# Kernel tuning notes

Measured on AMD Instinct MI355X. Metric: run time of the kernel, lower is better.

Reference implementation:

```python
import jax, jax.numpy as jnp
import numpy as np

B, L, E, H = 2, 2048, 1024, 16
D = E // H

def setup_inputs() -> dict:
    key = jax.random.key(0)
    ks = jax.random.split(key, 6)
    s = 1.0 / np.sqrt(E)
    return {
        "x": jax.random.normal(ks[0], (B, L, E), dtype=jnp.float32),
        "attention_mask": jnp.ones((B, L), dtype=jnp.float32),
        "Wq": jax.random.normal(ks[1], (E, E), dtype=jnp.float32) * s,
        "Wk": jax.random.normal(ks[2], (E, E), dtype=jnp.float32) * s,
        "Wv": jax.random.normal(ks[3], (E, E), dtype=jnp.float32) * s,
        "Wo": jax.random.normal(ks[4], (E, E), dtype=jnp.float32) * s,
        "bo": jnp.zeros((E,), dtype=jnp.float32),
    }

def reference(x, attention_mask, Wq, Wk, Wv, Wo, bo):
    b, l, e = x.shape
    h, d = H, D

    def proj(W):
        # (B,L,E) @ (E,E)^T -> (B,L,E) -> (B,H,L,D)
        return (x @ W.T).reshape(b, l, h, d).transpose(0, 2, 1, 3)

    q, k, v = proj(Wq), proj(Wk), proj(Wv)

    # multiplicative attention mask on q, k, v (mask shape (B,L) -> (B,1,L,1))
    m = attention_mask[:, None, :, None].astype(x.dtype)
    q, k, v = q * m, k * m, v * m

    scale = 1.0 / np.sqrt(d)
    scores = jnp.einsum('bhqd,bhkd->bhqk', q, k) * scale  # (B,H,L,L)
    causal = jnp.tril(jnp.ones((l, l), dtype=bool))
    scores = jnp.where(causal[None, None], scores, -jnp.inf)
    attn = jax.nn.softmax(scores, axis=-1)
    y = jnp.einsum('bhqk,bhkd->bhqd', attn, v)  # (B,H,L,D)
    y = y.transpose(0, 2, 1, 3).reshape(b, l, e)
    return y @ Wo.T + bo
```

## Files before the change

kernel.cpp:

```cpp
#include <hip/hip_runtime.h>
#include <cstdint>
#include <cstddef>
#include <math.h>

#define BB 2
#define LL 2048
#define EE 1024
#define HH 16
#define DD 64
#define MM (BB*LL)

typedef short short8 __attribute__((ext_vector_type(8)));
typedef float f32x4 __attribute__((ext_vector_type(4)));
typedef float f32x16 __attribute__((ext_vector_type(16)));

#define GPTR __attribute__((address_space(1)))
#define LPTR __attribute__((address_space(3)))

__device__ __forceinline__ unsigned pk_bf16(float lo, float hi) {
  unsigned r;
  asm("v_cvt_pk_bf16_f32 %0, %1, %2" : "=v"(r) : "v"(lo), "v"(hi));
  return r;
}
__device__ __forceinline__ unsigned short f32_bf16(float f) {
  return (unsigned short)pk_bf16(f, f);
}
__device__ __forceinline__ float ex2(float x) {
  float r;
  asm("v_exp_f32 %0, %1" : "=v"(r) : "v"(x));
  return r;
}
__device__ __forceinline__ void swap32(unsigned &a, unsigned &b) {
  asm("v_permlane32_swap_b32 %0, %1" : "+v"(a), "+v"(b));
}
__device__ __forceinline__ float xh_max(float v) {
  union { float f; unsigned u; } a, b;
  a.f = v;
  asm("v_mov_b32 %0, %1" : "=&v"(b.u) : "v"(a.u));
  asm("v_permlane32_swap_b32 %0, %1" : "+v"(a.u), "+v"(b.u));
  return fmaxf(a.f, b.f);
}
__device__ __forceinline__ float xh_sum(float v) {
  union { float f; unsigned u; } a, b;
  a.f = v;
  asm("v_mov_b32 %0, %1" : "=&v"(b.u) : "v"(a.u));
  asm("v_permlane32_swap_b32 %0, %1" : "+v"(a.u), "+v"(b.u));
  return a.f + b.f;
}
__device__ __forceinline__ f32x16 zero16() {
  f32x16 v;
  #pragma unroll
  for (int e = 0; e < 16; ++e) v[e] = 0.f;
  return v;
}

__global__ void cvt_all(const float* __restrict__ x,  const float* __restrict__ wq,
                        const float* __restrict__ wk, const float* __restrict__ wv,
                        const float* __restrict__ wo,
                        unsigned short* __restrict__ xb,  unsigned short* __restrict__ wqb,
                        unsigned short* __restrict__ wkb, unsigned short* __restrict__ wvb,
                        unsigned short* __restrict__ wob)
{
  int i = (blockIdx.x * 256 + threadIdx.x) * 4;
  if (i >= MM * EE + 4 * EE * EE) return;
  const float* s; unsigned short* d; int off;
  if (i < MM * EE) { s = x; d = xb; off = i; }
  else {
    int k = i - MM * EE;
    int w = k >> 20;
    off = k & (EE * EE - 1);
    s = (w == 0) ? wq : (w == 1) ? wk : (w == 2) ? wv : wo;
    d = (w == 0) ? wqb : (w == 1) ? wkb : (w == 2) ? wvb : wob;
  }
  float4 v = *(const float4*)(s + off);
  uint2 o;
  o.x = pk_bf16(v.x, v.y);
  o.y = pk_bf16(v.z, v.w);
  *(uint2*)(d + off) = o;
}

template<int MODE>
__global__ __launch_bounds__(256, 3)
void gemm128(const unsigned short* __restrict__ A,
             const unsigned short* __restrict__ W0,
             const unsigned short* __restrict__ W1,
             const unsigned short* __restrict__ W2,
             const float* __restrict__ mask,
             const float* __restrict__ bias,
             unsigned short* __restrict__ O0,
             unsigned short* __restrict__ O1,
             unsigned short* __restrict__ O2,
             float* __restrict__ OF)
{
  constexpr int K = EE;
  const int tid = threadIdx.x;
  const int lane = tid & 63;
  const int wid = tid >> 6;
  const int g = lane >> 4, li = lane & 15;
  const int m0 = blockIdx.y * 128;
  const int n0 = blockIdx.x * 128;
  const int z = blockIdx.z;

  const unsigned short* Wp = W0;
  if (MODE == 0) Wp = (z == 0) ? W0 : ((z == 1) ? W1 : W2);

  __shared__ unsigned short As[128 * 64];
  __shared__ unsigned short Bs[128 * 64];

  f32x4 acc[4][4];
  f32x4 zero = {0.f, 0.f, 0.f, 0.f};
  #pragma unroll
  for (int i = 0; i < 4; ++i)
    #pragma unroll
    for (int j = 0; j < 4; ++j) acc[i][j] = zero;

  const int wm = (wid >> 1) * 64;
  const int wn = (wid & 1) * 64;

  for (int kt = 0; kt < K; kt += 64) {
    #pragma unroll
    for (int j = 0; j < 4; ++j) {
      int c = j * 256 + tid;
      int row = c >> 3;
      int lcol = ((c & 7) * 16) ^ ((row & 7) << 4);
      __builtin_amdgcn_global_load_lds(
        (const GPTR void*)((const char*)(A + (size_t)(m0 + row) * K + kt) + lcol),
        (LPTR void*)((char*)As + c * 16), 16, 0, 0);
      __builtin_amdgcn_global_load_lds(
        (const GPTR void*)((const char*)(Wp + (size_t)(n0 + row) * K + kt) + lcol),
        (LPTR void*)((char*)Bs + c * 16), 16, 0, 0);
    }
    __syncthreads();

    #pragma unroll
    for (int kk = 0; kk < 2; ++kk) {
      short8 a[4], b[4];
      const int colb = (kk * 32 + g * 8) * 2;
      #pragma unroll
      for (int i = 0; i < 4; ++i) {
        int ar = wm + i * 16 + li;
        a[i] = *(const short8*)((const char*)As + ar * 128 + (colb ^ ((ar & 7) << 4)));
        int br = wn + i * 16 + li;
        b[i] = *(const short8*)((const char*)Bs + br * 128 + (colb ^ ((br & 7) << 4)));
      }
      #pragma unroll
      for (int i = 0; i < 4; ++i)
        #pragma unroll
        for (int j = 0; j < 4; ++j)
          acc[i][j] = __builtin_amdgcn_mfma_f32_16x16x32_bf16(a[i], b[j], acc[i][j], 0, 0, 0);
    }
    __syncthreads();
  }

  if (MODE == 0) {
    if (z == 2) {
      #pragma unroll
      for (int i = 0; i < 4; ++i) {
        int mbase = m0 + wm + i * 16 + g * 4;
        int bb2 = mbase >> 11;
        int l0  = mbase & (LL - 1);
        float mk[4];
        #pragma unroll
        for (int r = 0; r < 4; ++r) mk[r] = mask[mbase + r];
        #pragma unroll
        for (int j = 0; j < 4; ++j) {
          int n = n0 + wn + j * 16 + li;
          int h2 = n >> 6, dd2 = n & 63;
          uint2 o;
          o.x = pk_bf16(acc[i][j][0] * mk[0], acc[i][j][1] * mk[1]);
          o.y = pk_bf16(acc[i][j][2] * mk[2], acc[i][j][3] * mk[3]);
          size_t off = (size_t)(bb2 * HH + h2) * (LL * DD)
                     + (size_t)(l0 >> 5) * (DD * 32) + dd2 * 32 + (l0 & 31);
          *(uint2*)(O2 + off) = o;
        }
      }
    } else {
      unsigned short* Op = (z == 0) ? O0 : O1;
      const float sc = (z == 0) ? 0.125f * 1.44269504088896f : 1.0f;
      #pragma unroll
      for (int i = 0; i < 4; ++i) {
        #pragma unroll
        for (int r = 0; r < 4; ++r) {
          int m = m0 + wm + i * 16 + g * 4 + r;
          float mk = mask[m] * sc;
          int bb = m >> 11;
          int l  = m & (LL - 1);
          #pragma unroll
          for (int j = 0; j < 4; ++j) {
            int n = n0 + wn + j * 16 + li;
            int h = n >> 6, d = n & 63;
            size_t off = (((size_t)(bb * HH + h)) * LL + l) * DD + d;
            Op[off] = f32_bf16(acc[i][j][r] * mk);
          }
        }
      }
    }
  } else {
    #pragma unroll
    for (int i = 0; i < 4; ++i) {
      #pragma unroll
      for (int j = 0; j < 4; ++j) {
        int n = n0 + wn + j * 16 + li;
        float bv = bias[n];
        #pragma unroll
        for (int r = 0; r < 4; ++r) {
          int m = m0 + wm + i * 16 + g * 4 + r;
          OF[(size_t)m * EE + n] = acc[i][j][r] + bv;
        }
      }
    }
  }
}

__global__ __launch_bounds__(128, 2)
void attn11(const unsigned short* __restrict__ Q,
            const unsigned short* __restrict__ K,
            const unsigned short* __restrict__ VT,
            unsigned short* __restrict__ Y)
{
  const int tid = threadIdx.x, lane = tid & 63, w = tid >> 6;
  const int l31 = lane & 31, hi = lane >> 5;

  const int id = blockIdx.x;
  const int lo = id & 7;
  const int r_ = id >> 3;
  const int bh = (r_ & 3) * 8 + lo;
  const int p  = r_ >> 2;
  const int qth = 63 - p;
  const int qtl = p;
  const int b = bh >> 4, h = bh & (HH - 1);
  const size_t kbase = (size_t)bh * LL * DD;

  const unsigned short* Kg  = K + kbase;
  const unsigned short* VTg = VT + kbase;

  const int qrh = qth * 32 + l31;
  const int qrl = qtl * 32 + l31;

  short8 qfh[4], qfl[4];
  {
    const unsigned short* Qr = Q + kbase + (size_t)qrh * DD + hi * 8;
    #pragma unroll
    for (int kc = 0; kc < 4; ++kc) qfh[kc] = *(const short8*)(Qr + kc * 16);
    const unsigned short* Qs = Q + kbase + (size_t)qrl * DD + hi * 8;
    #pragma unroll
    for (int kc = 0; kc < 4; ++kc) qfl[kc] = *(const short8*)(Qs + kc * 16);
  }

  const f32x16 kZero = zero16();
  f32x16 oh0 = zero16(), oh1 = zero16(), ol0 = zero16(), ol1 = zero16();
  float mh = -INFINITY, ml = -INFINITY;
  float lsh4[4] = {0.f, 0.f, 0.f, 0.f};
  float lsl4[4] = {0.f, 0.f, 0.f, 0.f};

  short8 kA[4], vA[4], kB[4], vB[4];

  auto loadtile = [&](short8 (&kk)[4], short8 (&vv)[4], int t2) {
    const int kv0 = t2 << 5;
    const unsigned short* Kp = Kg + ((size_t)(kv0 + l31) << 6) + hi * 8;
    #pragma unroll
    for (int kc = 0; kc < 4; ++kc) kk[kc] = *(const short8*)(Kp + kc * 16);
    const unsigned short* Vp = VTg + (size_t)(kv0 >> 5) * (DD * 32) + l31 * 32 + hi * 8;
    vv[0] = *(const short8*)(Vp);
    vv[1] = *(const short8*)(Vp + 16);
    vv[2] = *(const short8*)(Vp + 32 * 32);
    vv[3] = *(const short8*)(Vp + 32 * 32 + 16);
  };

  loadtile(kA, vA, w);

  auto qk = [&](const short8 (&ck)[4], const short8 (&qf)[4]) -> f32x16 {
    f32x16 s0 = __builtin_amdgcn_mfma_f32_32x32x16_bf16(ck[0], qf[0], kZero, 0, 0, 0);
    f32x16 s1 = __builtin_amdgcn_mfma_f32_32x32x16_bf16(ck[1], qf[1], kZero, 0, 0, 0);
    s0 = __builtin_amdgcn_mfma_f32_32x32x16_bf16(ck[2], qf[2], s0, 0, 0, 0);
    s1 = __builtin_amdgcn_mfma_f32_32x32x16_bf16(ck[3], qf[3], s1, 0, 0, 0);
    #pragma unroll
    for (int e = 0; e < 16; ++e) s0[e] += s1[e];
    return s0;
  };

  auto diagmask = [&](f32x16 &s) {
    #pragma unroll
    for (int i = 0; i < 16; ++i) {
      int kvr = (i & 3) + 8 * (i >> 2) + 4 * hi;
      if (kvr > l31) s[i] = -INFINITY;
    }
  };

  auto process = [&](f32x16 &s, const short8 (&cv)[4],
                     float &mq, float (&ls4)[4], f32x16 &o0, f32x16 &o1) {
    float r0 = fmaxf(fmaxf(fmaxf(s[0], s[8]),  fmaxf(s[1], s[9])),  fmaxf(s[2], s[10]));
    float r1 = fmaxf(fmaxf(fmaxf(s[3], s[11]), fmaxf(s[4], s[12])), fmaxf(s[5], s[13]));
    float r2 = fmaxf(fmaxf(s[6], s[14]), fmaxf(s[7], s[15]));
    float mv = fmaxf(fmaxf(r0, r1), r2);

    if (!__all(mv <= mq + 8.0f)) {
      float mnew = fmaxf(mq, xh_max(mv));
      float al = ex2(mq - mnew);
      mq = mnew;
      #pragma unroll
      for (int e = 0; e < 16; ++e) { o0[e] *= al; o1[e] *= al; }
      #pragma unroll
      for (int e = 0; e < 4; ++e) ls4[e] *= al;
    }

    #pragma unroll
    for (int e = 0; e < 16; ++e) s[e] = ex2(s[e] - mq);
    ls4[0] += (s[0] + s[8])  + (s[4] + s[12]);
    ls4[1] += (s[1] + s[9])  + (s[5] + s[13]);
    ls4[2] += (s[2] + s[10]) + (s[6] + s[14]);
    ls4[3] += (s[3] + s[11]) + (s[7] + s[15]);

    auto mkfrag = [&](int base) -> short8 {
      unsigned a0 = pk_bf16(s[base + 0], s[base + 1]);
      unsigned a1 = pk_bf16(s[base + 2], s[base + 3]);
      unsigned b0 = pk_bf16(s[base + 4], s[base + 5]);
      unsigned b1 = pk_bf16(s[base + 6], s[base + 7]);
      swap32(a0, b0);
      swap32(a1, b1);
      union { unsigned u[4]; short8 s8; } f;
      f.u[0] = a0; f.u[1] = a1; f.u[2] = b0; f.u[3] = b1;
      return f.s8;
    };
    short8 pf0 = mkfrag(0), pf1 = mkfrag(8);

    o0 = __builtin_amdgcn_mfma_f32_32x32x16_bf16(cv[0], pf0, o0, 0, 0, 0);
    o1 = __builtin_amdgcn_mfma_f32_32x32x16_bf16(cv[2], pf0, o1, 0, 0, 0);
    o0 = __builtin_amdgcn_mfma_f32_32x32x16_bf16(cv[1], pf1, o0, 0, 0, 0);
    o1 = __builtin_amdgcn_mfma_f32_32x32x16_bf16(cv[3], pf1, o1, 0, 0, 0);
  };

  auto body = [&](short8 (&ck)[4], short8 (&cv)[4],
                  short8 (&nk)[4], short8 (&nv)[4], int t) {
    if (t + 2 <= qth) loadtile(nk, nv, t + 2);

    if (t <= qtl) {
      f32x16 sh = qk(ck, qfh);
      f32x16 sl = qk(ck, qfl);
      if (t == qtl) diagmask(sl);
      process(sh, cv, mh, lsh4, oh0, oh1);
      process(sl, cv, ml, lsl4, ol0, ol1);
    } else {
      f32x16 sh = qk(ck, qfh);
      if (t == qth) diagmask(sh);
      process(sh, cv, mh, lsh4, oh0, oh1);
    }
  };

  for (int t = w; t <= qth; t += 4) {
    body(kA, vA, kB, vB, t);
    if (t + 2 <= qth) body(kB, vB, kA, vA, t + 2);
  }

  float lsh = (lsh4[0] + lsh4[1]) + (lsh4[2] + lsh4[3]);
  float lsl = (lsl4[0] + lsl4[1]) + (lsl4[2] + lsl4[3]);

  __shared__ float mg[2][64][34];
  if (w == 1) {
    mg[0][lane][0] = mh; mg[0][lane][1] = lsh;
    mg[1][lane][0] = ml; mg[1][lane][1] = lsl;
    #pragma unroll
    for (int e = 0; e < 16; ++e) {
      mg[0][lane][2 + e] = oh0[e]; mg[0][lane][18 + e] = oh1[e];
      mg[1][lane][2 + e] = ol0[e]; mg[1][lane][18 + e] = ol1[e];
    }
  }
  __syncthreads();
  if (w == 0) {
    #pragma unroll
    for (int q = 0; q < 2; ++q) {
      float mw = (q == 0) ? mh : ml;
      float lw = (q == 0) ? lsh : lsl;
      const f32x16& o0 = (q == 0) ? oh0 : ol0;
      const f32x16& o1 = (q == 0) ? oh1 : ol1;
      int qrow = (q == 0) ? qrh : qrl;
      float m1 = mg[q][lane][0], l1 = mg[q][lane][1];
      float M = fmaxf(mw, m1);
      float a0 = ex2(fmaxf(mw - M, -200.0f));
      float a1 = ex2(fmaxf(m1 - M, -200.0f));
      float LtH = lw * a0 + l1 * a1;
      float Lt = xh_sum(LtH);
      float inv = 1.0f / Lt;
      unsigned short* Yr = Y + ((size_t)b * LL + qrow) * EE + h * DD;
      #pragma unroll
      for (int rg = 0; rg < 4; ++rg) {
        uint2 u0, u1;
        int i = rg * 4;
        u0.x = pk_bf16((o0[i]     * a0 + mg[q][lane][2 + i]     * a1) * inv,
                       (o0[i + 1] * a0 + mg[q][lane][3 + i]     * a1) * inv);
        u0.y = pk_bf16((o0[i + 2] * a0 + mg[q][lane][4 + i]     * a1) * inv,
                       (o0[i + 3] * a0 + mg[q][lane][5 + i]     * a1) * inv);
        u1.x = pk_bf16((o1[i]     * a0 + mg[q][lane][18 + i]    * a1) * inv,
                       (o1[i + 1] * a0 + mg[q][lane][19 + i]    * a1) * inv);
        u1.y = pk_bf16((o1[i + 2] * a0 + mg[q][lane][20 + i]    * a1) * inv,
                       (o1[i + 3] * a0 + mg[q][lane][21 + i]    * a1) * inv);
        *(uint2*)(Yr + rg * 8 + hi * 4) = u0;
        *(uint2*)(Yr + 32 + rg * 8 + hi * 4) = u1;
      }
    }
  }
}

extern "C" void kernel_launch(void* const* d_in, const int* in_sizes, int n_in,
                              void* d_out, int out_size, void* d_ws, size_t ws_size,
                              hipStream_t stream) {
  const float* x    = (const float*)d_in[0];
  const float* mask = (const float*)d_in[1];
  const float* Wq   = (const float*)d_in[2];
  const float* Wk   = (const float*)d_in[3];
  const float* Wv   = (const float*)d_in[4];
  const float* Wo   = (const float*)d_in[5];
  const float* bo   = (const float*)d_in[6];
  float* out = (float*)d_out;

  char* ws = (char*)d_ws;
  unsigned short* xb  = (unsigned short*)(ws);
  unsigned short* wqb = (unsigned short*)(ws + ((size_t)8  << 20));
  unsigned short* wkb = (unsigned short*)(ws + ((size_t)10 << 20));
  unsigned short* wvb = (unsigned short*)(ws + ((size_t)12 << 20));
  unsigned short* wob = (unsigned short*)(ws + ((size_t)14 << 20));
  unsigned short* Qb  = (unsigned short*)(ws + ((size_t)16 << 20));
  unsigned short* Kb  = (unsigned short*)(ws + ((size_t)24 << 20));
  unsigned short* VTb = (unsigned short*)(ws + ((size_t)32 << 20));
  unsigned short* Yb  = (unsigned short*)(ws + ((size_t)40 << 20));

  cvt_all<<<8192, 256, 0, stream>>>(x, Wq, Wk, Wv, Wo, xb, wqb, wkb, wvb, wob);

  gemm128<0><<<dim3(EE / 128, MM / 128, 3), 256, 0, stream>>>(
      xb, wqb, wkb, wvb, mask, nullptr, Qb, Kb, VTb, nullptr);

  attn11<<<dim3(1024), 128, 0, stream>>>(Qb, Kb, VTb, Yb);

  gemm128<1><<<dim3(EE / 128, MM / 128, 1), 256, 0, stream>>>(
      Yb, wob, nullptr, nullptr, nullptr, bo, nullptr, nullptr, nullptr, out);
}
```

Measured before the change: 107.4 us.

## Process two KV tiles per softmax update and split K/V prefetch in attention

The attention loop now handles the two KV tiles (t and t+2) together for the high query row. It does one combined max check and rescale, then issues eight PV MFMAs back to back. K and V loads for the next pair are split and placed around the softmax work, so K arrives before V is needed and loads overlap the exp/MFMA work. This halves the online-softmax rescale checks for the long row and deepens prefetch. The cost is more live registers (two score tiles plus four fragment sets), which may add register pressure under the 2-wave launch bound.

```diff
diff --git a/kernel.cpp b/kernel.cpp
--- a/kernel.cpp
+++ b/kernel.cpp
@@ -213,7 +213,7 @@
 }
 
 __global__ __launch_bounds__(128, 2)
-void attn11(const unsigned short* __restrict__ Q,
+void attn14(const unsigned short* __restrict__ Q,
             const unsigned short* __restrict__ K,
             const unsigned short* __restrict__ VT,
             unsigned short* __restrict__ Y)
@@ -255,11 +255,14 @@
 
   short8 kA[4], vA[4], kB[4], vB[4];
 
-  auto loadtile = [&](short8 (&kk)[4], short8 (&vv)[4], int t2) {
+  auto loadK = [&](short8 (&kk)[4], int t2) {
     const int kv0 = t2 << 5;
     const unsigned short* Kp = Kg + ((size_t)(kv0 + l31) << 6) + hi * 8;
     #pragma unroll
     for (int kc = 0; kc < 4; ++kc) kk[kc] = *(const short8*)(Kp + kc * 16);
+  };
+  auto loadV = [&](short8 (&vv)[4], int t2) {
+    const int kv0 = t2 << 5;
     const unsigned short* Vp = VTg + (size_t)(kv0 >> 5) * (DD * 32) + l31 * 32 + hi * 8;
     vv[0] = *(const short8*)(Vp);
     vv[1] = *(const short8*)(Vp + 16);
@@ -267,8 +270,6 @@
     vv[3] = *(const short8*)(Vp + 32 * 32 + 16);
   };
 
-  loadtile(kA, vA, w);
-
   auto qk = [&](const short8 (&ck)[4], const short8 (&qf)[4]) -> f32x16 {
     f32x16 s0 = __builtin_amdgcn_mfma_f32_32x32x16_bf16(ck[0], qf[0], kZero, 0, 0, 0);
     f32x16 s1 = __builtin_amdgcn_mfma_f32_32x32x16_bf16(ck[1], qf[1], kZero, 0, 0, 0);
@@ -287,13 +288,28 @@
     }
   };
 
-  auto process = [&](f32x16 &s, const short8 (&cv)[4],
-                     float &mq, float (&ls4)[4], f32x16 &o0, f32x16 &o1) {
+  auto localmax = [&](const f32x16 &s) -> float {
     float r0 = fmaxf(fmaxf(fmaxf(s[0], s[8]),  fmaxf(s[1], s[9])),  fmaxf(s[2], s[10]));
     float r1 = fmaxf(fmaxf(fmaxf(s[3], s[11]), fmaxf(s[4], s[12])), fmaxf(s[5], s[13]));
     float r2 = fmaxf(fmaxf(s[6], s[14]), fmaxf(s[7], s[15]));
-    float mv = fmaxf(fmaxf(r0, r1), r2);
-
+    return fmaxf(fmaxf(r0, r1), r2);
+  };
+
+  auto mkfrag = [&](const f32x16 &s, int base) -> short8 {
+    unsigned a0 = pk_bf16(s[base + 0], s[base + 1]);
+    unsigned a1 = pk_bf16(s[base + 2], s[base + 3]);
+    unsigned b0 = pk_bf16(s[base + 4], s[base + 5]);
+    unsigned b1 = pk_bf16(s[base + 6], s[base + 7]);
+    swap32(a0, b0);
+    swap32(a1, b1);
+    union { unsigned u[4]; short8 s8; } f;
+    f.u[0] = a0; f.u[1] = a1; f.u[2] = b0; f.u[3] = b1;
+    return f.s8;
+  };
+
+  auto process = [&](f32x16 &s, const short8 (&cv)[4],
+                     float &mq, float (&ls4)[4], f32x16 &o0, f32x16 &o1) {
+    float mv = localmax(s);
     if (!__all(mv <= mq + 8.0f)) {
       float mnew = fmaxf(mq, xh_max(mv));
       float al = ex2(mq - mnew);
@@ -303,53 +319,87 @@
       #pragma unroll
       for (int e = 0; e < 4; ++e) ls4[e] *= al;
     }
-
     #pragma unroll
     for (int e = 0; e < 16; ++e) s[e] = ex2(s[e] - mq);
     ls4[0] += (s[0] + s[8])  + (s[4] + s[12]);
     ls4[1] += (s[1] + s[9])  + (s[5] + s[13]);
     ls4[2] += (s[2] + s[10]) + (s[6] + s[14]);
     ls4[3] += (s[3] + s[11]) + (s[7] + s[15]);
-
-    auto mkfrag = [&](int base) -> short8 {
-      unsigned a0 = pk_bf16(s[base + 0], s[base + 1]);
-      unsigned a1 = pk_bf16(s[base + 2], s[base + 3]);
-      unsigned b0 = pk_bf16(s[base + 4], s[base + 5]);
-      unsigned b1 = pk_bf16(s[base + 6], s[base + 7]);
-      swap32(a0, b0);
-      swap32(a1, b1);
-      union { unsigned u[4]; short8 s8; } f;
-      f.u[0] = a0; f.u[1] = a1; f.u[2] = b0; f.u[3] = b1;
-      return f.s8;
-    };
-    short8 pf0 = mkfrag(0), pf1 = mkfrag(8);
-
+    short8 pf0 = mkfrag(s, 0), pf1 = mkfrag(s, 8);
     o0 = __builtin_amdgcn_mfma_f32_32x32x16_bf16(cv[0], pf0, o0, 0, 0, 0);
     o1 = __builtin_amdgcn_mfma_f32_32x32x16_bf16(cv[2], pf0, o1, 0, 0, 0);
     o0 = __builtin_amdgcn_mfma_f32_32x32x16_bf16(cv[1], pf1, o0, 0, 0, 0);
     o1 = __builtin_amdgcn_mfma_f32_32x32x16_bf16(cv[3], pf1, o1, 0, 0, 0);
   };
 
-  auto body = [&](short8 (&ck)[4], short8 (&cv)[4],
-                  short8 (&nk)[4], short8 (&nv)[4], int t) {
-    if (t + 2 <= qth) loadtile(nk, nv, t + 2);
+  auto process2 = [&](f32x16 &sa, f32x16 &sb) {
+    float mv = fmaxf(localmax(sa), localmax(sb));
+    if (!__all(mv <= mh + 8.0f)) {
+      float mnew = fmaxf(mh, xh_max(mv));
+      float al = ex2(mh - mnew);
+      mh = mnew;
+      #pragma unroll
+      for (int e = 0; e < 16; ++e) { oh0[e] *= al; oh1[e] *= al; }
+      #pragma unroll
+      for (int e = 0; e < 4; ++e) lsh4[e] *= al;
+    }
+    #pragma unroll
+    for (int e = 0; e < 16; ++e) sa[e] = ex2(sa[e] - mh);
+    #pragma unroll
+    for (int e = 0; e < 16; ++e) sb[e] = ex2(sb[e] - mh);
+    lsh4[0] += (sa[0] + sa[8])  + (sa[4] + sa[12]) + (sb[0] + sb[8])  + (sb[4] + sb[12]);
+    lsh4[1] += (sa[1] + sa[9])  + (sa[5] + sa[13]) + (sb[1] + sb[9])  + (sb[5] + sb[13]);
+    lsh4[2] += (sa[2] + sa[10]) + (sa[6] + sa[14]) + (sb[2] + sb[10]) + (sb[6] + sb[14]);
+    lsh4[3] += (sa[3] + sa[11]) + (sa[7] + sa[15]) + (sb[3] + sb[11]) + (sb[7] + sb[15]);
+    short8 pa0 = mkfrag(sa, 0), pa1 = mkfrag(sa, 8);
+    short8 pb0 = mkfrag(sb, 0), pb1 = mkfrag(sb, 8);
+    oh0 = __builtin_amdgcn_mfma_f32_32x32x16_bf16(vA[0], pa0, oh0, 0, 0, 0);
+    oh1 = __builtin_amdgcn_mfma_f32_32x32x16_bf16(vA[2], pa0, oh1, 0, 0, 0);
+    oh0 = __builtin_amdgcn_mfma_f32_32x32x16_bf16(vA[1], pa1, oh0, 0, 0, 0);
+    oh1 = __builtin_amdgcn_mfma_f32_32x32x16_bf16(vA[3], pa1, oh1, 0, 0, 0);
+    oh0 = __builtin_amdgcn_mfma_f32_32x32x16_bf16(vB[0], pb0, oh0, 0, 0, 0);
+    oh1 = __builtin_amdgcn_mfma_f32_32x32x16_bf16(vB[2], pb0, oh1, 0, 0, 0);
+    oh0 = __builtin_amdgcn_mfma_f32_32x32x16_bf16(vB[1], pb1, oh0, 0, 0, 0);
+    oh1 = __builtin_amdgcn_mfma_f32_32x32x16_bf16(vB[3], pb1, oh1, 0, 0, 0);
+  };
+
+  loadK(kA, w);  loadV(vA, w);
+  loadK(kB, w + 2); loadV(vB, w + 2);
+
+  int t = w;
+  for (; t + 2 <= qth; t += 4) {
+    f32x16 sa = qk(kA, qfh);
+    f32x16 sb = qk(kB, qfh);
+    if (t + 2 == qth) diagmask(sb);
 
     if (t <= qtl) {
-      f32x16 sh = qk(ck, qfh);
-      f32x16 sl = qk(ck, qfl);
+      f32x16 sl = qk(kA, qfl);
       if (t == qtl) diagmask(sl);
-      process(sh, cv, mh, lsh4, oh0, oh1);
-      process(sl, cv, ml, lsl4, ol0, ol1);
-    } else {
-      f32x16 sh = qk(ck, qfh);
-      if (t == qth) diagmask(sh);
-      process(sh, cv, mh, lsh4, oh0, oh1);
-    }
-  };
-
-  for (int t = w; t <= qth; t += 4) {
-    body(kA, vA, kB, vB, t);
-    if (t + 2 <= qth) body(kB, vB, kA, vA, t + 2);
+      process(sl, vA, ml, lsl4, ol0, ol1);
+    }
+    if (t + 2 <= qtl) {
+      f32x16 sl = qk(kB, qfl);
+      if (t + 2 == qtl) diagmask(sl);
+      process(sl, vB, ml, lsl4, ol0, ol1);
+    }
+
+    if (t + 4 <= qth) loadK(kA, t + 4);
+    if (t + 6 <= qth) loadK(kB, t + 6);
+
+    process2(sa, sb);
+
+    if (t + 4 <= qth) loadV(vA, t + 4);
+    if (t + 6 <= qth) loadV(vB, t + 6);
+  }
+  if (t <= qth) {
+    f32x16 sh = qk(kA, qfh);
+    if (t == qth) diagmask(sh);
+    if (t <= qtl) {
+      f32x16 sl = qk(kA, qfl);
+      if (t == qtl) diagmask(sl);
+      process(sl, vA, ml, lsl4, ol0, ol1);
+    }
+    process(sh, vA, mh, lsh4, oh0, oh1);
   }
 
   float lsh = (lsh4[0] + lsh4[1]) + (lsh4[2] + lsh4[3]);
@@ -386,14 +436,14 @@
       for (int rg = 0; rg < 4; ++rg) {
         uint2 u0, u1;
         int i = rg * 4;
-        u0.x = pk_bf16((o0[i]     * a0 + mg[q][lane][2 + i]     * a1) * inv,
-                       (o0[i + 1] * a0 + mg[q][lane][3 + i]     * a1) * inv);
-        u0.y = pk_bf16((o0[i + 2] * a0 + mg[q][lane][4 + i]     * a1) * inv,
-                       (o0[i + 3] * a0 + mg[q][lane][5 + i]     * a1) * inv);
-        u1.x = pk_bf16((o1[i]     * a0 + mg[q][lane][18 + i]    * a1) * inv,
-                       (o1[i + 1] * a0 + mg[q][lane][19 + i]    * a1) * inv);
-        u1.y = pk_bf16((o1[i + 2] * a0 + mg[q][lane][20 + i]    * a1) * inv,
-                       (o1[i + 3] * a0 + mg[q][lane][21 + i]    * a1) * inv);
+        u0.x = pk_bf16((o0[i]     * a0 + mg[q][lane][2 + i]  * a1) * inv,
+                       (o0[i + 1] * a0 + mg[q][lane][3 + i]  * a1) * inv);
+        u0.y = pk_bf16((o0[i + 2] * a0 + mg[q][lane][4 + i]  * a1) * inv,
+                       (o0[i + 3] * a0 + mg[q][lane][5 + i]  * a1) * inv);
+        u1.x = pk_bf16((o1[i]     * a0 + mg[q][lane][18 + i] * a1) * inv,
+                       (o1[i + 1] * a0 + mg[q][lane][19 + i] * a1) * inv);
+        u1.y = pk_bf16((o1[i + 2] * a0 + mg[q][lane][20 + i] * a1) * inv,
+                       (o1[i + 3] * a0 + mg[q][lane][21 + i] * a1) * inv);
         *(uint2*)(Yr + rg * 8 + hi * 4) = u0;
         *(uint2*)(Yr + 32 + rg * 8 + hi * 4) = u1;
       }
@@ -429,7 +479,7 @@
   gemm128<0><<<dim3(EE / 128, MM / 128, 3), 256, 0, stream>>>(
       xb, wqb, wkb, wvb, mask, nullptr, Qb, Kb, VTb, nullptr);
 
-  attn11<<<dim3(1024), 128, 0, stream>>>(Qb, Kb, VTb, Yb);
+  attn14<<<dim3(1024), 128, 0, stream>>>(Qb, Kb, VTb, Yb);
 
   gemm128<1><<<dim3(EE / 128, MM / 128, 1), 256, 0, stream>>>(
       Yb, wob, nullptr, nullptr, nullptr, bo, nullptr, nullptr, nullptr, out);
```

New measurement: 111.7 us. 1.04x slower.
